# Optimization experiments

Hardware: AMD Instinct MI355X
Metric: run time of the kernel (lower is better)

The kernel has to match this reference:

```python
import jax, jax.numpy as jnp
import numpy as np

G, N = 1024, 40            # graphs, nodes per graph (complete graphs)
SLOPE = 0.1                # leaky relu negative slope
SMAT_IDX = jnp.array([0, 1, 2, 3, 1, 4, 5, 6, 2, 5, 7, 8, 3, 6, 8, 9])


def setup_inputs() -> dict:
    key = jax.random.key(0)
    ks = jax.random.split(key, 24)

    # --- graph structure: G identical complete graphs of N nodes ---
    ii, jj = np.meshgrid(np.arange(N), np.arange(N), indexing="ij")
    mask = ii != jj
    src_l, dst_l = ii[mask], jj[mask]              # directed edges per graph
    offs = (np.arange(G) * N)[:, None]
    edge_index = np.stack([(src_l[None] + offs).ravel(),
                           (dst_l[None] + offs).ravel()]).astype(np.int64)
    iu, ju = np.triu_indices(N, 1)
    M = iu.shape[0]                                 # 780 undirected edges
    ud_edges = np.stack([iu, ju], 1).astype(np.int64)
    edge_map = np.zeros((N, N), np.int64)
    edge_map[iu, ju] = np.arange(M)
    edge_map[ju, iu] = np.arange(M)

    def w(k, shape, fan_in):
        return jax.random.normal(k, shape, jnp.float32) / np.sqrt(fan_in)

    inp = {
        "x": jax.random.normal(ks[0], (G * N, 16), jnp.float32),
        "edge_index": jnp.asarray(edge_index),
        "ud_edges": jnp.asarray(ud_edges),
        "edge_map": jnp.asarray(edge_map),
        # GCN stack 6->32->32->64
        "Wg0": w(ks[1], (6, 32), 6),   "bg0": jnp.zeros((32,), jnp.float32),
        "Wg1": w(ks[2], (32, 32), 32), "bg1": jnp.zeros((32,), jnp.float32),
        "Wg2": w(ks[3], (32, 64), 32), "bg2": jnp.zeros((64,), jnp.float32),
        # node MLP 64->64->64->10
        "Wn0": w(ks[4], (64, 64), 64), "bn0": jnp.zeros((64,), jnp.float32),
        "Wn1": w(ks[5], (64, 64), 64), "bn1": jnp.zeros((64,), jnp.float32),
        "Wn2": w(ks[6], (64, 10), 64), "bn2": jnp.zeros((10,), jnp.float32),
        # edge MLP 64->64->64->10
        "We0": w(ks[7], (64, 64), 64), "be0": jnp.zeros((64,), jnp.float32),
        "We1": w(ks[8], (64, 64), 64), "be1": jnp.zeros((64,), jnp.float32),
        "We2": w(ks[9], (64, 10), 64), "be2": jnp.zeros((10,), jnp.float32),
    }
    return inp


def _forward(x, edge_index, ud_edges, edge_map,
             Wg0, bg0, Wg1, bg1, Wg2, bg2,
             Wn0, bn0, Wn1, bn1, Wn2, bn2,
             We0, be0, We1, be1, We2, be2):
    num_nodes = x.shape[0]
    h = x[:, :6]                                   # node_feature_mode == 1
    src, dst = edge_index[0], edge_index[1]

    # GCN normalization (add_self_loops=False, edge_weight=1)
    deg = jax.ops.segment_sum(jnp.ones(src.shape[0], x.dtype), dst,
                              num_segments=num_nodes)
    dis = jnp.where(deg > 0, jax.lax.rsqrt(jnp.maximum(deg, 1e-12)), 0.0)
    norm = dis[src] * dis[dst]                     # [E]

    def gcn(h, W, b):
        m = (h @ W)[src] * norm[:, None]
        return jax.ops.segment_sum(m, dst, num_segments=num_nodes) + b

    # eval mode: dropout is identity
    h = jax.nn.leaky_relu(gcn(h, Wg0, bg0), SLOPE)
    h = jax.nn.leaky_relu(gcn(h, Wg1, bg1), SLOPE)
    h = gcn(h, Wg2, bg2)                           # [G*N, 64]

    hg = h.reshape(G, N, -1)                       # [G, N, 64]

    def mlp(z, Ws, bs):
        for W, b in zip(Ws[:-1], bs[:-1]):
            z = jax.nn.leaky_relu(z @ W + b, SLOPE)
        return z @ Ws[-1] + bs[-1]

    vp = mlp(hg, [Wn0, Wn1, Wn2], [bn0, bn1, bn2])            # [G, N, 10]
    e = hg[:, ud_edges[:, 0], :] + hg[:, ud_edges[:, 1], :]   # [G, M, 64]
    ep = mlp(e, [We0, We1, We2], [be0, be1, be2])             # [G, M, 10]

    # recover_X: diag blocks smat(vp[i]), off-diag smat(ep[edge_map[i,j]])
    epm = ep[:, edge_map, :]                                  # [G, N, N, 10]
    eye = jnp.eye(N, dtype=bool)[None, :, :, None]
    vecs = jnp.where(eye, vp[:, :, None, :], epm)             # [G, N, N, 10]
    blocks = vecs[..., SMAT_IDX].reshape(G, N, N, 4, 4)
    X = blocks.transpose(0, 1, 3, 2, 4).reshape(G, 4 * N, 4 * N)
    return h, X


def reference(x, edge_index, ud_edges, edge_map,
              Wg0, bg0, Wg1, bg1, Wg2, bg2,
              Wn0, bn0, Wn1, bn1, Wn2, bn2,
              We0, be0, We1, be1, We2, be2):
    return _forward(x, edge_index, ud_edges, edge_map,
                    Wg0, bg0, Wg1, bg1, Wg2, bg2,
                    Wn0, bn0, Wn1, bn1, Wn2, bn2,
                    We0, be0, We1, be1, We2, be2)
```

## Files before the change

kernel.cpp:

```cpp
#include <hip/hip_runtime.h>

#define G_GRAPHS 1024
#define N_NODES  40
#define M_EDGES  780
#define NUM_NODES (G_GRAPHS * N_NODES)
#define H_ELEMS  (NUM_NODES * 64)
#define X_STRIDE 160
#define X_PER_G  25600
#define SLOPE 0.1f

#define PACK_PER_MLP 9216

typedef __bf16 bf16x8 __attribute__((ext_vector_type(8)));
typedef unsigned short us8 __attribute__((ext_vector_type(8)));
typedef float f32x4 __attribute__((ext_vector_type(4)));

__device__ __forceinline__ float lrelu(float v) { return fmaxf(v, SLOPE * v); }
__device__ __forceinline__ unsigned short f2bf(float x) {
    __bf16 b = (__bf16)x;
    return __builtin_bit_cast(unsigned short, b);
}
__device__ __forceinline__ unsigned int pk2bf(float a, float b) {
    return (unsigned int)f2bf(a) | ((unsigned int)f2bf(b) << 16);
}

__global__ __launch_bounds__(256) void k_prep(const float* __restrict__ We0,
                                              const float* __restrict__ We1,
                                              const float* __restrict__ We2,
                                              const float* __restrict__ Wn0,
                                              const float* __restrict__ Wn1,
                                              const float* __restrict__ Wn2,
                                              unsigned short* __restrict__ wp) {
    int t = blockIdx.x * 256 + threadIdx.x;
    int mlp = t / PACK_PER_MLP;
    int o = t - mlp * PACK_PER_MLP;
    const float* W0 = mlp ? Wn0 : We0;
    const float* W1 = mlp ? Wn1 : We1;
    const float* W2 = mlp ? Wn2 : We2;
    float val;
    if (o < 8192) {
        const float* W = (o < 4096) ? W0 : W1;
        int idx = o & 4095;
        int j = idx & 7, l = (idx >> 3) & 63, tt = idx >> 9;
        int kt = tt & 1, mt = tt >> 1;
        int k = kt * 32 + ((l >> 4) & 3) * 8 + j;
        int m = mt * 16 + (l & 15);
        val = W[k * 64 + m];
    } else {
        int idx = o - 8192;
        int j = idx & 7, l = (idx >> 3) & 63, kt = idx >> 9;
        int k = kt * 32 + ((l >> 4) & 3) * 8 + j;
        int m = l & 15;
        val = (m < 10) ? W2[k * 10 + m] : 0.f;
    }
    wp[mlp * PACK_PER_MLP + o] = f2bf(val);
}

__global__ __launch_bounds__(256, 4) void k_gcn(const float* __restrict__ x,
                                                const float* __restrict__ Wg0,
                                                const float* __restrict__ bg0,
                                                const float* __restrict__ Wg1,
                                                const float* __restrict__ bg1,
                                                const float* __restrict__ Wg2,
                                                const float* __restrict__ bg2,
                                                float* __restrict__ hout) {
    __shared__ __align__(16) float h0[N_NODES * 6];
    __shared__ __align__(16) float buf[N_NODES * 64];
    __shared__ float S[64];
    __shared__ float P[8 * 64];
    __shared__ __align__(16) float h1[N_NODES * 32];
    __shared__ __align__(16) float h2[N_NODES * 32];

    const int g = blockIdx.x;
    const int tid = threadIdx.x;
    const float inv39 = 1.0f / 39.0f;
    const int c32 = tid & 31;
    const int c64 = tid & 63;

    float w0c[6], w1c[32], w2c[32];
#pragma unroll
    for (int f = 0; f < 6; f++)  w0c[f] = Wg0[f * 32 + c32];
#pragma unroll
    for (int m = 0; m < 32; m++) w1c[m] = Wg1[m * 32 + c32];
#pragma unroll
    for (int m = 0; m < 32; m++) w2c[m] = Wg2[m * 64 + c64];
    const float b0c = bg0[c32];
    const float b1c = bg1[c32];
    const float b2c = bg2[c64];

    for (int idx = tid; idx < N_NODES * 6; idx += 256) {
        int n = idx / 6, f = idx - n * 6;
        h0[idx] = x[(g * N_NODES + n) * 16 + f];
    }
    __syncthreads();

    {
        int n0 = tid >> 5;
#pragma unroll
        for (int t = 0; t < 5; t++) {
            int n = n0 + 8 * t;
            float s = 0.f;
#pragma unroll
            for (int f = 0; f < 6; f++) s += h0[n * 6 + f] * w0c[f];
            buf[n * 32 + c32] = s;
        }
    }
    __syncthreads();
    { int grp = tid >> 5; float s = 0.f;
#pragma unroll
      for (int n = grp * 5; n < grp * 5 + 5; n++) s += buf[n * 32 + c32];
      P[grp * 32 + c32] = s; }
    __syncthreads();
    if (tid < 32) { float s = 0.f;
#pragma unroll
      for (int grp = 0; grp < 8; grp++) s += P[grp * 32 + tid];
      S[tid] = s; }
    __syncthreads();
    for (int idx = tid; idx < N_NODES * 32; idx += 256)
        h1[idx] = lrelu((S[c32] - buf[idx]) * inv39 + b0c);
    __syncthreads();

    {
        int n0 = tid >> 5;
#pragma unroll
        for (int t = 0; t < 5; t++) {
            int n = n0 + 8 * t;
            const float4* hp = (const float4*)(h1 + n * 32);
            float s = 0.f;
#pragma unroll
            for (int q = 0; q < 8; q++) {
                float4 hv = hp[q];
                s += hv.x * w1c[4 * q + 0] + hv.y * w1c[4 * q + 1]
                   + hv.z * w1c[4 * q + 2] + hv.w * w1c[4 * q + 3];
            }
            buf[n * 32 + c32] = s;
        }
    }
    __syncthreads();
    { int grp = tid >> 5; float s = 0.f;
#pragma unroll
      for (int n = grp * 5; n < grp * 5 + 5; n++) s += buf[n * 32 + c32];
      P[grp * 32 + c32] = s; }
    __syncthreads();
    if (tid < 32) { float s = 0.f;
#pragma unroll
      for (int grp = 0; grp < 8; grp++) s += P[grp * 32 + tid];
      S[tid] = s; }
    __syncthreads();
    for (int idx = tid; idx < N_NODES * 32; idx += 256)
        h2[idx] = lrelu((S[c32] - buf[idx]) * inv39 + b1c);
    __syncthreads();

    {
        int n0 = tid >> 6;
#pragma unroll
        for (int t = 0; t < 10; t++) {
            int n = n0 + 4 * t;
            const float4* hp = (const float4*)(h2 + n * 32);
            float s = 0.f;
#pragma unroll
            for (int q = 0; q < 8; q++) {
                float4 hv = hp[q];
                s += hv.x * w2c[4 * q + 0] + hv.y * w2c[4 * q + 1]
                   + hv.z * w2c[4 * q + 2] + hv.w * w2c[4 * q + 3];
            }
            buf[n * 64 + c64] = s;
        }
    }
    __syncthreads();
    { int grp = tid >> 6; float s = 0.f;
#pragma unroll
      for (int n = grp * 10; n < grp * 10 + 10; n++) s += buf[n * 64 + c64];
      P[grp * 64 + c64] = s; }
    __syncthreads();
    if (tid < 64) { float s = 0.f;
#pragma unroll
      for (int grp = 0; grp < 4; grp++) s += P[grp * 64 + tid];
      S[tid] = s; }
    __syncthreads();
    for (int idx = tid; idx < N_NODES * 64; idx += 256)
        hout[g * N_NODES * 64 + idx] = (S[c64] - buf[idx]) * inv39 + b2c;
}

struct ChunkRegs {
    bf16x8 A1[4][2];
    bf16x8 A2[4][2];
    bf16x8 A3[2];
    float4 bv0[4];
    float4 bv1[4];
    float  bz[4];
};

__device__ __forceinline__ void run_chunk(int R0, int w, int l,
                                          const float4* sh4,
                                          unsigned short* sB,
                                          float* sEP,
                                          const ChunkRegs& cr) {
    const int nl = l & 15;
    const int rq = (l >> 4) & 3;

    {
        int rl = l >> 1, hf2 = l & 1;
        int row = R0 + rl;
        int ii = 0, jj = 0;
        bool addf = false;
        if (row < 780) {
            float tq = 6241.0f - 8.0f * (float)row;
            int i0 = (int)(0.5f * (79.0f - sqrtf(tq)));
            i0 = min(38, max(0, i0));
            int cum = 39 * i0 - ((i0 * (i0 - 1)) >> 1);
            if (cum > row) { --i0; cum = 39 * i0 - ((i0 * (i0 - 1)) >> 1); }
            else if (row - cum >= 39 - i0) { cum += 39 - i0; ++i0; }
            ii = i0; jj = i0 + 1 + (row - cum);
            addf = true;
        } else if (row >= 800 && row < 840) {
            ii = jj = row - 800;
        }
        unsigned short tmp[32];
#pragma unroll
        for (int q = 0; q < 8; q++) {
            int u = hf2 * 8 + q;
            float4 a = sh4[ii * 16 + (u ^ ((ii & 7) << 1))];
            if (addf) {
                float4 bq = sh4[jj * 16 + (u ^ ((jj & 7) << 1))];
                a.x += bq.x; a.y += bq.y; a.z += bq.z; a.w += bq.w;
            }
            tmp[4 * q + 0] = f2bf(a.x); tmp[4 * q + 1] = f2bf(a.y);
            tmp[4 * q + 2] = f2bf(a.z); tmp[4 * q + 3] = f2bf(a.w);
        }
        int r_sb = 32 * w + rl;
#pragma unroll
        for (int q = 0; q < 4; q++) {
            int cs = (hf2 * 4 + q) ^ (r_sb & 7);
            *(us8*)((char*)sB + r_sb * 128 + cs * 16) = *(const us8*)(tmp + 8 * q);
        }
    }

    auto ZB = [&](int nt, int kt) -> bf16x8 {
        int node = 32 * w + nt * 16 + nl;
        int cs = (kt * 4 + rq) ^ (node & 7);
        return __builtin_bit_cast(bf16x8,
            *(const us8*)((const char*)sB + node * 128 + cs * 16));
    };
    auto zstore = [&](int mt, int nt, const f32x4& v) {
        int node = 32 * w + nt * 16 + nl;
        int cs = (mt * 2 + (rq >> 1)) ^ (node & 7);
        uint2 u = make_uint2(pk2bf(v[0], v[1]), pk2bf(v[2], v[3]));
        *(uint2*)((char*)sB + node * 128 + cs * 16 + (rq & 1) * 8) = u;
    };

    {
        bf16x8 B[2][2];
#pragma unroll
        for (int nt = 0; nt < 2; nt++)
#pragma unroll
            for (int kt = 0; kt < 2; kt++) B[nt][kt] = ZB(nt, kt);
#pragma unroll
        for (int mt = 0; mt < 4; mt++) {
            float4 bv = cr.bv0[mt];
#pragma unroll
            for (int nt = 0; nt < 2; nt++) {
                f32x4 acc = (f32x4){0.f, 0.f, 0.f, 0.f};
                acc = __builtin_amdgcn_mfma_f32_16x16x32_bf16(cr.A1[mt][0], B[nt][0], acc, 0, 0, 0);
                acc = __builtin_amdgcn_mfma_f32_16x16x32_bf16(cr.A1[mt][1], B[nt][1], acc, 0, 0, 0);
                f32x4 z;
                z[0] = lrelu(acc[0] + bv.x); z[1] = lrelu(acc[1] + bv.y);
                z[2] = lrelu(acc[2] + bv.z); z[3] = lrelu(acc[3] + bv.w);
                zstore(mt, nt, z);
            }
        }
    }

    {
        bf16x8 B[2][2];
#pragma unroll
        for (int nt = 0; nt < 2; nt++)
#pragma unroll
            for (int kt = 0; kt < 2; kt++) B[nt][kt] = ZB(nt, kt);
#pragma unroll
        for (int mt = 0; mt < 4; mt++) {
            float4 bv = cr.bv1[mt];
#pragma unroll
            for (int nt = 0; nt < 2; nt++) {
                f32x4 acc = (f32x4){0.f, 0.f, 0.f, 0.f};
                acc = __builtin_amdgcn_mfma_f32_16x16x32_bf16(cr.A2[mt][0], B[nt][0], acc, 0, 0, 0);
                acc = __builtin_amdgcn_mfma_f32_16x16x32_bf16(cr.A2[mt][1], B[nt][1], acc, 0, 0, 0);
                f32x4 z;
                z[0] = lrelu(acc[0] + bv.x); z[1] = lrelu(acc[1] + bv.y);
                z[2] = lrelu(acc[2] + bv.z); z[3] = lrelu(acc[3] + bv.w);
                zstore(mt, nt, z);
            }
        }
    }

    {
        bf16x8 B[2][2];
#pragma unroll
        for (int nt = 0; nt < 2; nt++)
#pragma unroll
            for (int kt = 0; kt < 2; kt++) B[nt][kt] = ZB(nt, kt);
#pragma unroll
        for (int nt = 0; nt < 2; nt++) {
            f32x4 acc = (f32x4){0.f, 0.f, 0.f, 0.f};
            acc = __builtin_amdgcn_mfma_f32_16x16x32_bf16(cr.A3[0], B[nt][0], acc, 0, 0, 0);
            acc = __builtin_amdgcn_mfma_f32_16x16x32_bf16(cr.A3[1], B[nt][1], acc, 0, 0, 0);
            int rowe = R0 + nt * 16 + nl;
            bool valid = (rowe < 780) || (rowe >= 800 && rowe < 840);
            if (valid && rq < 3) {
                int epr = (rowe < 780) ? rowe : rowe - 20;
                float* p = sEP + epr * 10 + rq * 4;
                *(float2*)p = make_float2(acc[0] + cr.bz[0], acc[1] + cr.bz[1]);
                if (rq < 2)
                    *(float2*)(p + 2) = make_float2(acc[2] + cr.bz[2], acc[3] + cr.bz[3]);
            }
        }
    }
}

__global__ __launch_bounds__(256) void k_mlp(const float* __restrict__ h,
                                             const unsigned short* __restrict__ wp,
                                             const float* __restrict__ be0,
                                             const float* __restrict__ be1,
                                             const float* __restrict__ be2,
                                             const float* __restrict__ bn0,
                                             const float* __restrict__ bn1,
                                             const float* __restrict__ bn2,
                                             float* __restrict__ X) {
    __shared__ __align__(16) float sh[N_NODES * 64];
    __shared__ __align__(16) unsigned short sB[128 * 64];
    __shared__ __align__(8)  float sEP[820 * 10];

    const int tid = threadIdx.x;
    const int l = tid & 63;
    const int w = tid >> 6;
    const int g = blockIdx.x;
    const int rq = (l >> 4) & 3;

    float4* sh4 = (float4*)sh;

    {
        const float4* hg4 = (const float4*)(h + g * (N_NODES * 64));
#pragma unroll
        for (int k = 0; k < 3; k++) {
            int v = k * 256 + tid;
            if (v < 640) {
                int i = v >> 4, u = v & 15;
                sh4[i * 16 + (u ^ ((i & 7) << 1))] = hg4[v];
            }
        }
    }

    auto WA = [&](const unsigned short* base, int mt, int kt) -> bf16x8 {
        return __builtin_bit_cast(bf16x8,
            *(const us8*)(base + ((mt * 2 + kt) * 64 + l) * 8));
    };

    ChunkRegs ce;
#pragma unroll
    for (int mt = 0; mt < 4; mt++) {
#pragma unroll
        for (int kt = 0; kt < 2; kt++) {
            ce.A1[mt][kt] = WA(wp, mt, kt);
            ce.A2[mt][kt] = WA(wp + 4096, mt, kt);
        }
        ce.bv0[mt] = *(const float4*)(be0 + mt * 16 + rq * 4);
        ce.bv1[mt] = *(const float4*)(be1 + mt * 16 + rq * 4);
    }
    ce.A3[0] = WA(wp + 8192, 0, 0);
    ce.A3[1] = WA(wp + 8192, 0, 1);
#pragma unroll
    for (int k = 0; k < 4; k++) {
        int f = rq * 4 + k;
        ce.bz[k] = (f < 10) ? be2[f] : 0.f;
    }

    __syncthreads();

    for (int c = w; c < 27; c += 4) {
        if (c < 25) {
            run_chunk(c * 32, w, l, sh4, sB, sEP, ce);
        } else {
            const unsigned short* wn = wp + PACK_PER_MLP;
            ChunkRegs cn;
#pragma unroll
            for (int mt = 0; mt < 4; mt++) {
#pragma unroll
                for (int kt = 0; kt < 2; kt++) {
                    cn.A1[mt][kt] = WA(wn, mt, kt);
                    cn.A2[mt][kt] = WA(wn + 4096, mt, kt);
                }
                cn.bv0[mt] = *(const float4*)(bn0 + mt * 16 + rq * 4);
                cn.bv1[mt] = *(const float4*)(bn1 + mt * 16 + rq * 4);
            }
            cn.A3[0] = WA(wn + 8192, 0, 0);
            cn.A3[1] = WA(wn + 8192, 0, 1);
#pragma unroll
            for (int k = 0; k < 4; k++) {
                int f = rq * 4 + k;
                cn.bz[k] = (f < 10) ? bn2[f] : 0.f;
            }
            run_chunk(c * 32, w, l, sh4, sB, sEP, cn);
        }
    }

    __syncthreads();

    float* Xg = X + g * X_PER_G;
#pragma unroll
    for (int k = 0; k < 7; k++) {
        int b = k * 256 + tid;
        if (b < 1600) {
            int bi = b / 40;
            int bj = b - bi * 40;
            int ridx;
            if (bi == bj) {
                ridx = 780 + bi;
            } else {
                int mn = min(bi, bj), mx = max(bi, bj);
                ridx = 39 * mn - ((mn * (mn - 1)) >> 1) + (mx - mn - 1);
            }
            const float* ep = sEP + ridx * 10;
            float2 e0 = *(const float2*)(ep + 0);
            float2 e1 = *(const float2*)(ep + 2);
            float2 e2 = *(const float2*)(ep + 4);
            float2 e3 = *(const float2*)(ep + 6);
            float2 e4 = *(const float2*)(ep + 8);
            float f0 = e0.x, f1 = e0.y, f2 = e1.x, f3 = e1.y;
            float f4 = e2.x, f5 = e2.y, f6 = e3.x, f7 = e3.y;
            float f8 = e4.x, f9 = e4.y;
            float4 r0 = make_float4(f0, f1, f2, f3);
            float4 r1 = make_float4(f1, f4, f5, f6);
            float4 r2 = make_float4(f2, f5, f7, f8);
            float4 r3 = make_float4(f3, f6, f8, f9);
            float* p = Xg + (4 * bi) * X_STRIDE + 4 * bj;
            *(float4*)(p + 0 * X_STRIDE) = r0;
            *(float4*)(p + 1 * X_STRIDE) = r1;
            *(float4*)(p + 2 * X_STRIDE) = r2;
            *(float4*)(p + 3 * X_STRIDE) = r3;
        }
    }
}

extern "C" void kernel_launch(void* const* d_in, const int* in_sizes, int n_in,
                              void* d_out, int out_size, void* d_ws, size_t ws_size,
                              hipStream_t stream) {
    const float* x   = (const float*)d_in[0];
    const float* Wg0 = (const float*)d_in[4];
    const float* bg0 = (const float*)d_in[5];
    const float* Wg1 = (const float*)d_in[6];
    const float* bg1 = (const float*)d_in[7];
    const float* Wg2 = (const float*)d_in[8];
    const float* bg2 = (const float*)d_in[9];
    const float* Wn0 = (const float*)d_in[10];
    const float* bn0 = (const float*)d_in[11];
    const float* Wn1 = (const float*)d_in[12];
    const float* bn1 = (const float*)d_in[13];
    const float* Wn2 = (const float*)d_in[14];
    const float* bn2 = (const float*)d_in[15];
    const float* We0 = (const float*)d_in[16];
    const float* be0 = (const float*)d_in[17];
    const float* We1 = (const float*)d_in[18];
    const float* be1 = (const float*)d_in[19];
    const float* We2 = (const float*)d_in[20];
    const float* be2 = (const float*)d_in[21];

    float* hout = (float*)d_out;
    float* X    = hout + H_ELEMS;
    unsigned short* wp = (unsigned short*)d_ws;

    k_prep<<<72, 256, 0, stream>>>(We0, We1, We2, Wn0, Wn1, Wn2, wp);
    k_gcn<<<G_GRAPHS, 256, 0, stream>>>(x, Wg0, bg0, Wg1, bg1, Wg2, bg2, hout);
    k_mlp<<<G_GRAPHS, 256, 0, stream>>>(hout, wp,
                                        be0, be1, be2,
                                        bn0, bn1, bn2, X);
}
```

Baseline: 233.0 us.

## Fuse GCN and MLP kernels into one per-graph kernel with aliased shared memory

```diff
diff --git a/kernel.cpp b/kernel.cpp
--- a/kernel.cpp
+++ b/kernel.cpp
@@ -56,132 +56,6 @@
     wp[mlp * PACK_PER_MLP + o] = f2bf(val);
 }
 
-__global__ __launch_bounds__(256, 4) void k_gcn(const float* __restrict__ x,
-                                                const float* __restrict__ Wg0,
-                                                const float* __restrict__ bg0,
-                                                const float* __restrict__ Wg1,
-                                                const float* __restrict__ bg1,
-                                                const float* __restrict__ Wg2,
-                                                const float* __restrict__ bg2,
-                                                float* __restrict__ hout) {
-    __shared__ __align__(16) float h0[N_NODES * 6];
-    __shared__ __align__(16) float buf[N_NODES * 64];
-    __shared__ float S[64];
-    __shared__ float P[8 * 64];
-    __shared__ __align__(16) float h1[N_NODES * 32];
-    __shared__ __align__(16) float h2[N_NODES * 32];
-
-    const int g = blockIdx.x;
-    const int tid = threadIdx.x;
-    const float inv39 = 1.0f / 39.0f;
-    const int c32 = tid & 31;
-    const int c64 = tid & 63;
-
-    float w0c[6], w1c[32], w2c[32];
-#pragma unroll
-    for (int f = 0; f < 6; f++)  w0c[f] = Wg0[f * 32 + c32];
-#pragma unroll
-    for (int m = 0; m < 32; m++) w1c[m] = Wg1[m * 32 + c32];
-#pragma unroll
-    for (int m = 0; m < 32; m++) w2c[m] = Wg2[m * 64 + c64];
-    const float b0c = bg0[c32];
-    const float b1c = bg1[c32];
-    const float b2c = bg2[c64];
-
-    for (int idx = tid; idx < N_NODES * 6; idx += 256) {
-        int n = idx / 6, f = idx - n * 6;
-        h0[idx] = x[(g * N_NODES + n) * 16 + f];
-    }
-    __syncthreads();
-
-    {
-        int n0 = tid >> 5;
-#pragma unroll
-        for (int t = 0; t < 5; t++) {
-            int n = n0 + 8 * t;
-            float s = 0.f;
-#pragma unroll
-            for (int f = 0; f < 6; f++) s += h0[n * 6 + f] * w0c[f];
-            buf[n * 32 + c32] = s;
-        }
-    }
-    __syncthreads();
-    { int grp = tid >> 5; float s = 0.f;
-#pragma unroll
-      for (int n = grp * 5; n < grp * 5 + 5; n++) s += buf[n * 32 + c32];
-      P[grp * 32 + c32] = s; }
-    __syncthreads();
-    if (tid < 32) { float s = 0.f;
-#pragma unroll
-      for (int grp = 0; grp < 8; grp++) s += P[grp * 32 + tid];
-      S[tid] = s; }
-    __syncthreads();
-    for (int idx = tid; idx < N_NODES * 32; idx += 256)
-        h1[idx] = lrelu((S[c32] - buf[idx]) * inv39 + b0c);
-    __syncthreads();
-
-    {
-        int n0 = tid >> 5;
-#pragma unroll
-        for (int t = 0; t < 5; t++) {
-            int n = n0 + 8 * t;
-            const float4* hp = (const float4*)(h1 + n * 32);
-            float s = 0.f;
-#pragma unroll
-            for (int q = 0; q < 8; q++) {
-                float4 hv = hp[q];
-                s += hv.x * w1c[4 * q + 0] + hv.y * w1c[4 * q + 1]
-                   + hv.z * w1c[4 * q + 2] + hv.w * w1c[4 * q + 3];
-            }
-            buf[n * 32 + c32] = s;
-        }
-    }
-    __syncthreads();
-    { int grp = tid >> 5; float s = 0.f;
-#pragma unroll
-      for (int n = grp * 5; n < grp * 5 + 5; n++) s += buf[n * 32 + c32];
-      P[grp * 32 + c32] = s; }
-    __syncthreads();
-    if (tid < 32) { float s = 0.f;
-#pragma unroll
-      for (int grp = 0; grp < 8; grp++) s += P[grp * 32 + tid];
-      S[tid] = s; }
-    __syncthreads();
-    for (int idx = tid; idx < N_NODES * 32; idx += 256)
-        h2[idx] = lrelu((S[c32] - buf[idx]) * inv39 + b1c);
-    __syncthreads();
-
-    {
-        int n0 = tid >> 6;
-#pragma unroll
-        for (int t = 0; t < 10; t++) {
-            int n = n0 + 4 * t;
-            const float4* hp = (const float4*)(h2 + n * 32);
-            float s = 0.f;
-#pragma unroll
-            for (int q = 0; q < 8; q++) {
-                float4 hv = hp[q];
-                s += hv.x * w2c[4 * q + 0] + hv.y * w2c[4 * q + 1]
-                   + hv.z * w2c[4 * q + 2] + hv.w * w2c[4 * q + 3];
-            }
-            buf[n * 64 + c64] = s;
-        }
-    }
-    __syncthreads();
-    { int grp = tid >> 6; float s = 0.f;
-#pragma unroll
-      for (int n = grp * 10; n < grp * 10 + 10; n++) s += buf[n * 64 + c64];
-      P[grp * 64 + c64] = s; }
-    __syncthreads();
-    if (tid < 64) { float s = 0.f;
-#pragma unroll
-      for (int grp = 0; grp < 4; grp++) s += P[grp * 64 + tid];
-      S[tid] = s; }
-    __syncthreads();
-    for (int idx = tid; idx < N_NODES * 64; idx += 256)
-        hout[g * N_NODES * 64 + idx] = (S[c64] - buf[idx]) * inv39 + b2c;
-}
-
 struct ChunkRegs {
     bf16x8 A1[4][2];
     bf16x8 A2[4][2];
@@ -317,38 +191,157 @@
     }
 }
 
-__global__ __launch_bounds__(256) void k_mlp(const float* __restrict__ h,
-                                             const unsigned short* __restrict__ wp,
-                                             const float* __restrict__ be0,
-                                             const float* __restrict__ be1,
-                                             const float* __restrict__ be2,
-                                             const float* __restrict__ bn0,
-                                             const float* __restrict__ bn1,
-                                             const float* __restrict__ bn2,
-                                             float* __restrict__ X) {
-    __shared__ __align__(16) float sh[N_NODES * 64];
-    __shared__ __align__(16) unsigned short sB[128 * 64];
-    __shared__ __align__(8)  float sEP[820 * 10];
-
+__global__ __launch_bounds__(256, 2) void k_fused(const float* __restrict__ x,
+                                                  const float* __restrict__ Wg0,
+                                                  const float* __restrict__ bg0,
+                                                  const float* __restrict__ Wg1,
+                                                  const float* __restrict__ bg1,
+                                                  const float* __restrict__ Wg2,
+                                                  const float* __restrict__ bg2,
+                                                  const unsigned short* __restrict__ wp,
+                                                  const float* __restrict__ be0,
+                                                  const float* __restrict__ be1,
+                                                  const float* __restrict__ be2,
+                                                  const float* __restrict__ bn0,
+                                                  const float* __restrict__ bn1,
+                                                  const float* __restrict__ bn2,
+                                                  float* __restrict__ hout,
+                                                  float* __restrict__ X) {
+    __shared__ __align__(16) char smem[59424];
+    float* sh            = (float*)smem;
+    unsigned short* sB   = (unsigned short*)(smem + 10240);
+    float* sEP           = (float*)(smem + 26624);
+    float* buf = (float*)(smem + 10240);
+    float* h1  = (float*)(smem + 20480);
+    float* h2  = (float*)(smem + 25600);
+    float* h0  = (float*)(smem + 30720);
+    float* P   = (float*)(smem + 31744);
+    float* S   = (float*)(smem + 33792);
+
+    const int g = blockIdx.x;
     const int tid = threadIdx.x;
     const int l = tid & 63;
     const int w = tid >> 6;
-    const int g = blockIdx.x;
+    const float inv39 = 1.0f / 39.0f;
+    const int c32 = tid & 31;
+    const int c64 = tid & 63;
     const int rq = (l >> 4) & 3;
 
-    float4* sh4 = (float4*)sh;
-
     {
-        const float4* hg4 = (const float4*)(h + g * (N_NODES * 64));
-#pragma unroll
-        for (int k = 0; k < 3; k++) {
-            int v = k * 256 + tid;
-            if (v < 640) {
-                int i = v >> 4, u = v & 15;
-                sh4[i * 16 + (u ^ ((i & 7) << 1))] = hg4[v];
-            }
-        }
-    }
+        float w0c[6], w1c[32], w2c[32];
+#pragma unroll
+        for (int f = 0; f < 6; f++)  w0c[f] = Wg0[f * 32 + c32];
+#pragma unroll
+        for (int m = 0; m < 32; m++) w1c[m] = Wg1[m * 32 + c32];
+#pragma unroll
+        for (int m = 0; m < 32; m++) w2c[m] = Wg2[m * 64 + c64];
+        const float b0c = bg0[c32];
+        const float b1c = bg1[c32];
+        const float b2c = bg2[c64];
+
+        for (int idx = tid; idx < N_NODES * 6; idx += 256) {
+            int n = idx / 6, f = idx - n * 6;
+            h0[idx] = x[(g * N_NODES + n) * 16 + f];
+        }
+        __syncthreads();
+
+        {
+            int n0 = tid >> 5;
+#pragma unroll
+            for (int t = 0; t < 5; t++) {
+                int n = n0 + 8 * t;
+                float s = 0.f;
+#pragma unroll
+                for (int f = 0; f < 6; f++) s += h0[n * 6 + f] * w0c[f];
+                buf[n * 32 + c32] = s;
+            }
+        }
+        __syncthreads();
+        { int grp = tid >> 5; float s = 0.f;
+#pragma unroll
+          for (int n = grp * 5; n < grp * 5 + 5; n++) s += buf[n * 32 + c32];
+          P[grp * 32 + c32] = s; }
+        __syncthreads();
+        if (tid < 32) { float s = 0.f;
+#pragma unroll
+          for (int grp = 0; grp < 8; grp++) s += P[grp * 32 + tid];
+          S[tid] = s; }
+        __syncthreads();
+        for (int idx = tid; idx < N_NODES * 32; idx += 256)
+            h1[idx] = lrelu((S[c32] - buf[idx]) * inv39 + b0c);
+        __syncthreads();
+
+        {
+            int n0 = tid >> 5;
+#pragma unroll
+            for (int t = 0; t < 5; t++) {
+                int n = n0 + 8 * t;
+                const float4* hp = (const float4*)(h1 + n * 32);
+                float s = 0.f;
+#pragma unroll
+                for (int q = 0; q < 8; q++) {
+                    float4 hv = hp[q];
+                    s += hv.x * w1c[4 * q + 0] + hv.y * w1c[4 * q + 1]
+                       + hv.z * w1c[4 * q + 2] + hv.w * w1c[4 * q + 3];
+                }
+                buf[n * 32 + c32] = s;
+            }
+        }
+        __syncthreads();
+        { int grp = tid >> 5; float s = 0.f;
+#pragma unroll
+          for (int n = grp * 5; n < grp * 5 + 5; n++) s += buf[n * 32 + c32];
+          P[grp * 32 + c32] = s; }
+        __syncthreads();
+        if (tid < 32) { float s = 0.f;
+#pragma unroll
+          for (int grp = 0; grp < 8; grp++) s += P[grp * 32 + tid];
+          S[tid] = s; }
+        __syncthreads();
+        for (int idx = tid; idx < N_NODES * 32; idx += 256)
+            h2[idx] = lrelu((S[c32] - buf[idx]) * inv39 + b1c);
+        __syncthreads();
+
+        {
+            int n0 = tid >> 6;
+#pragma unroll
+            for (int t = 0; t < 10; t++) {
+                int n = n0 + 4 * t;
+                const float4* hp = (const float4*)(h2 + n * 32);
+                float s = 0.f;
+#pragma unroll
+                for (int q = 0; q < 8; q++) {
+                    float4 hv = hp[q];
+                    s += hv.x * w2c[4 * q + 0] + hv.y * w2c[4 * q + 1]
+                       + hv.z * w2c[4 * q + 2] + hv.w * w2c[4 * q + 3];
+                }
+                buf[n * 64 + c64] = s;
+            }
+        }
+        __syncthreads();
+        { int grp = tid >> 6; float s = 0.f;
+#pragma unroll
+          for (int n = grp * 10; n < grp * 10 + 10; n++) s += buf[n * 64 + c64];
+          P[grp * 64 + c64] = s; }
+        __syncthreads();
+        if (tid < 64) { float s = 0.f;
+#pragma unroll
+          for (int grp = 0; grp < 4; grp++) s += P[grp * 64 + tid];
+          S[tid] = s; }
+        __syncthreads();
+
+        for (int idx = tid; idx < N_NODES * 64; idx += 256) {
+            float v = (S[c64] - buf[idx]) * inv39 + b2c;
+            hout[g * N_NODES * 64 + idx] = v;
+            int n = idx >> 6;
+            int u = c64 >> 2;
+            int us = u ^ ((n & 7) << 1);
+            sh[n * 64 + us * 4 + (c64 & 3)] = v;
+        }
+    }
+    __syncthreads();
+
+    const float4* sh4 = (const float4*)sh;
 
     auto WA = [&](const unsigned short* base, int mt, int kt) -> bf16x8 {
         return __builtin_bit_cast(bf16x8,
@@ -373,8 +366,6 @@
         int f = rq * 4 + k;
         ce.bz[k] = (f < 10) ? be2[f] : 0.f;
     }
-
-    __syncthreads();
 
     for (int c = w; c < 27; c += 4) {
         if (c < 25) {
@@ -469,8 +460,7 @@
     unsigned short* wp = (unsigned short*)d_ws;
 
     k_prep<<<72, 256, 0, stream>>>(We0, We1, We2, Wn0, Wn1, Wn2, wp);
-    k_gcn<<<G_GRAPHS, 256, 0, stream>>>(x, Wg0, bg0, Wg1, bg1, Wg2, bg2, hout);
-    k_mlp<<<G_GRAPHS, 256, 0, stream>>>(hout, wp,
-                                        be0, be1, be2,
-                                        bn0, bn1, bn2, X);
-}
+    k_fused<<<G_GRAPHS, 256, 0, stream>>>(x, Wg0, bg0, Wg1, bg1, Wg2, bg2,
+                                          wp, be0, be1, be2, bn0, bn1, bn2,
+                                          hout, X);
+}
```

Measured after the change: 234.0 us. About the same (+0.4%).
